# Performance work log

Hardware: AMD Instinct MI355X
Metric: run time of the kernel (lower is better)

The kernel has to match this reference:

```python
import jax, jax.numpy as jnp
import numpy as np


def setup_inputs() -> dict:
    key = jax.random.key(0)
    ks = jax.random.split(key, 9)
    B, C, O, T, H, W = 2, 256, 256, 16, 64, 64
    fea_th = jax.random.normal(ks[0], (B, C, T, H), dtype=jnp.float32)
    fea_tw = jax.random.normal(ks[1], (B, C, T, W), dtype=jnp.float32)
    fea_obj = jax.random.normal(ks[2], (B, C, T), dtype=jnp.float32)
    heatmap = jax.random.uniform(ks[3], (B, 1, T, H, W), dtype=jnp.float32)
    mask = jax.random.uniform(ks[4], (B, 1, T, H, W), dtype=jnp.float32)
    s = 1.0 / np.sqrt(C)
    W3d = jax.random.uniform(ks[5], (O, C), dtype=jnp.float32, minval=-s, maxval=s)
    b3d = jax.random.uniform(ks[6], (O,), dtype=jnp.float32, minval=-s, maxval=s)
    W1d = jax.random.uniform(ks[7], (O, C), dtype=jnp.float32, minval=-s, maxval=s)
    b1d = jax.random.uniform(ks[8], (O,), dtype=jnp.float32, minval=-s, maxval=s)
    return {"fea_th": fea_th, "fea_tw": fea_tw, "fea_obj": fea_obj,
            "heatmap": heatmap, "mask": mask,
            "W3d": W3d, "b3d": b3d, "W1d": W1d, "b1d": b1d}


def reference(fea_th, fea_tw, fea_obj, heatmap, mask, W3d, b3d, W1d, b1d):
    # Outer product over spatial dims: [B,C,T,H,1] * [B,C,T,1,W] -> [B,C,T,H,W]
    out_fea = fea_th[..., None] * fea_tw[..., None, :]
    # 1x1x1 Conv3d == channel mixing: bcthw,oc -> bothw (+ bias)
    out_fea = jnp.einsum('bcthw,oc->bothw', out_fea, W3d) + b3d[None, :, None, None, None]
    # 1x1 Conv1d on fea_obj: bct,oc -> bot (+ bias), then broadcast over H,W
    fea_obj_ = (jnp.einsum('bct,oc->bot', fea_obj, W1d) + b1d[None, :, None])[..., None, None]
    # Heatmap blend and mask
    out_fea = out_fea * (1.0 - heatmap) + fea_obj_ * heatmap
    out_fea = out_fea * mask
    return out_fea
```

## Files before the change

kernel.cpp:

```cpp
#include <hip/hip_runtime.h>
#include <hip/hip_bf16.h>

#define B_ 2
#define C_ 256
#define O_ 256
#define T_ 16
#define H_ 64
#define W_ 64

typedef __bf16 bf16x8 __attribute__((ext_vector_type(8)));
typedef float  f32x4  __attribute__((ext_vector_type(4)));

#define WS_OBJ_OFF 131072

__global__ __launch_bounds__(256) void prep_kernel(
    const float* __restrict__ fea_obj, const float* __restrict__ W3d,
    const float* __restrict__ W1d, const float* __restrict__ b1d,
    __bf16* __restrict__ wsW, float* __restrict__ wsObj) {
    const int bid = blockIdx.x;
    const int tid = threadIdx.x;
    if (bid < 32) {
        const int b = bid >> 4, t = bid & 15;
        __shared__ float fo[C_];
        fo[tid] = fea_obj[(b * C_ + tid) * T_ + t];
        __syncthreads();
        const int o = tid;
        const float4* wrow = (const float4*)(W1d + o * C_);
        float s = 0.f;
#pragma unroll 8
        for (int cq = 0; cq < C_ / 4; ++cq) {
            float4 wv = wrow[cq];
            s += wv.x * fo[cq * 4 + 0] + wv.y * fo[cq * 4 + 1] +
                 wv.z * fo[cq * 4 + 2] + wv.w * fo[cq * 4 + 3];
        }
        wsObj[(b * T_ + t) * O_ + o] = s + b1d[o];
    } else {
        const int g = (bid - 32) * 256 + tid;
        const int o = g >> 5;
        const int cg = g & 31;
        const float* sp = W3d + o * C_ + cg * 8;
        float4 a0 = *(const float4*)sp;
        float4 a1 = *(const float4*)(sp + 4);
        bf16x8 pk;
        pk[0] = (__bf16)a0.x; pk[1] = (__bf16)a0.y;
        pk[2] = (__bf16)a0.z; pk[3] = (__bf16)a0.w;
        pk[4] = (__bf16)a1.x; pk[5] = (__bf16)a1.y;
        pk[6] = (__bf16)a1.z; pk[7] = (__bf16)a1.w;
        *(bf16x8*)((char*)wsW + o * 512 + cg * 16) = pk;
    }
}

__global__ __attribute__((amdgpu_flat_work_group_size(512, 512)))
void main_kernel(
    const float* __restrict__ fea_th, const float* __restrict__ fea_tw,
    const float* __restrict__ heatmap, const float* __restrict__ mask,
    const float* __restrict__ b3d,
    const __bf16* __restrict__ wsW, const float* __restrict__ wsObj,
    float* __restrict__ out) {
    __shared__ __align__(16) char smem[43008];
    char*  sB0  = smem;
    char*  sB1  = smem + 16384;
    float* sTh  = (float*)(smem + 32768);
    float* sPb  = (float*)(smem + 40960);
    float* sObj = (float*)(smem + 41984);

    const int tid  = threadIdx.x;
    const int lane = tid & 63;
    const int wv   = tid >> 6;
    const int kgrp = lane >> 4;
    const int l15  = lane & 15;

    const int bid = blockIdx.x;
    const int wb = bid & 1, hg = (bid >> 1) & 7, bt = bid >> 4;
    const int b = bt >> 4, t = bt & 15;
    const int h0 = hg * 8, w0 = wb * 32;

    const float* objp = wsObj + (b * T_ + t) * O_;
    if (tid < 256) {
        const float* thp = fea_th + ((b * C_ + tid) * T_ + t) * H_ + h0;
        float4 v0 = *(const float4*)thp;
        float4 v1 = *(const float4*)(thp + 4);
        sTh[0 * 256 + tid] = v0.x;  sTh[1 * 256 + tid] = v0.y;
        sTh[2 * 256 + tid] = v0.z;  sTh[3 * 256 + tid] = v0.w;
        sTh[4 * 256 + tid] = v1.x;  sTh[5 * 256 + tid] = v1.y;
        sTh[6 * 256 + tid] = v1.z;  sTh[7 * 256 + tid] = v1.w;
        sPb[tid]  = b3d[tid];
        sObj[tid] = objp[tid];
    }

    const int wl = tid & 31;
    const int cs = (tid >> 5) * 16;
    bf16x8 twb0, twb1;
    {
        const float* twp = fea_tw + ((b * C_ + cs) * T_ + t) * W_ + w0 + wl;
#pragma unroll
        for (int j = 0; j < 8; ++j) twb0[j] = (__bf16)twp[j * (T_ * W_)];
#pragma unroll
        for (int j = 0; j < 8; ++j) twb1[j] = (__bf16)twp[(8 + j) * (T_ * W_)];
    }

    bf16x8 af[2][8];
#pragma unroll
    for (int mf = 0; mf < 2; ++mf)
#pragma unroll
        for (int ks = 0; ks < 8; ++ks)
            af[mf][ks] = *(const bf16x8*)(
                wsW + (wv * 32 + mf * 16 + l15) * 256 + ks * 32 + kgrp * 8);

    const int swzW = (wl & 7) << 4;
    const int c0g  = (cs >> 3) * 16;

    auto build = [&](int hl, char* dst) {
        const float* thp = sTh + hl * 256 + cs;
        const f32x4 t0 = *(const f32x4*)thp;
        const f32x4 t1 = *(const f32x4*)(thp + 4);
        const f32x4 t2 = *(const f32x4*)(thp + 8);
        const f32x4 t3 = *(const f32x4*)(thp + 12);
        bf16x8 z0, z1;
        z0[0] = (__bf16)((float)twb0[0] * t0[0]);
        z0[1] = (__bf16)((float)twb0[1] * t0[1]);
        z0[2] = (__bf16)((float)twb0[2] * t0[2]);
        z0[3] = (__bf16)((float)twb0[3] * t0[3]);
        z0[4] = (__bf16)((float)twb0[4] * t1[0]);
        z0[5] = (__bf16)((float)twb0[5] * t1[1]);
        z0[6] = (__bf16)((float)twb0[6] * t1[2]);
        z0[7] = (__bf16)((float)twb0[7] * t1[3]);
        z1[0] = (__bf16)((float)twb1[0] * t2[0]);
        z1[1] = (__bf16)((float)twb1[1] * t2[1]);
        z1[2] = (__bf16)((float)twb1[2] * t2[2]);
        z1[3] = (__bf16)((float)twb1[3] * t2[3]);
        z1[4] = (__bf16)((float)twb1[4] * t3[0]);
        z1[5] = (__bf16)((float)twb1[5] * t3[1]);
        z1[6] = (__bf16)((float)twb1[6] * t3[2]);
        z1[7] = (__bf16)((float)twb1[7] * t3[3]);
        *(bf16x8*)(dst + wl * 512 + (c0g ^ swzW))        = z0;
        *(bf16x8*)(dst + wl * 512 + ((c0g + 16) ^ swzW)) = z1;
    };

    __syncthreads();
    build(0, sB0);
    __syncthreads();

    const int hmb  = (b * T_ + t) * (H_ * W_);
    const int swzR = (l15 & 7) << 4;
    const int ob0  = wv * 32 + kgrp * 4;

    for (int hl = 0; hl < 8; ++hl) {
        char* cur = (hl & 1) ? sB1 : sB0;
        if (hl < 7) build(hl + 1, (hl & 1) ? sB0 : sB1);

        const int hglb = h0 + hl;
        const int hrow = hmb + hglb * W_ + w0 + l15;
        const float ht0 = heatmap[hrow],      mk0 = mask[hrow];
        const float ht1 = heatmap[hrow + 16], mk1 = mask[hrow + 16];

        f32x4 acc[2][2] = {};
#pragma unroll
        for (int ks = 0; ks < 8; ++ks) {
            const int kb = ks * 64 + kgrp * 16;
            const bf16x8 b0 = *(const bf16x8*)(cur + l15 * 512 + (kb ^ swzR));
            const bf16x8 b1 = *(const bf16x8*)(cur + (16 + l15) * 512 + (kb ^ swzR));
            acc[0][0] = __builtin_amdgcn_mfma_f32_16x16x32_bf16(af[0][ks], b0, acc[0][0], 0, 0, 0);
            acc[0][1] = __builtin_amdgcn_mfma_f32_16x16x32_bf16(af[0][ks], b1, acc[0][1], 0, 0, 0);
            acc[1][0] = __builtin_amdgcn_mfma_f32_16x16x32_bf16(af[1][ks], b0, acc[1][0], 0, 0, 0);
            acc[1][1] = __builtin_amdgcn_mfma_f32_16x16x32_bf16(af[1][ks], b1, acc[1][1], 0, 0, 0);
        }

#pragma unroll
        for (int mf = 0; mf < 2; ++mf) {
            const f32x4 pb4 = *(const f32x4*)(sPb + ob0 + mf * 16);
            const f32x4 po4 = *(const f32x4*)(sObj + ob0 + mf * 16);
#pragma unroll
            for (int r = 0; r < 4; ++r) {
                const int o = ob0 + mf * 16 + r;
                float* orow = out + (((size_t)(b * O_ + o) * T_ + t) * H_ + hglb) * W_ + w0;
                float v0 = acc[mf][0][r] + pb4[r];
                v0 = v0 * (1.f - ht0) + po4[r] * ht0;
                orow[l15] = v0 * mk0;
                float v1 = acc[mf][1][r] + pb4[r];
                v1 = v1 * (1.f - ht1) + po4[r] * ht1;
                orow[16 + l15] = v1 * mk1;
            }
        }
        __syncthreads();
    }
}

extern "C" void kernel_launch(void* const* d_in, const int* in_sizes, int n_in,
                              void* d_out, int out_size, void* d_ws, size_t ws_size,
                              hipStream_t stream) {
    const float* fea_th  = (const float*)d_in[0];
    const float* fea_tw  = (const float*)d_in[1];
    const float* fea_obj = (const float*)d_in[2];
    const float* heatmap = (const float*)d_in[3];
    const float* mask    = (const float*)d_in[4];
    const float* W3d     = (const float*)d_in[5];
    const float* b3d     = (const float*)d_in[6];
    const float* W1d     = (const float*)d_in[7];
    const float* b1d     = (const float*)d_in[8];
    float* out = (float*)d_out;

    __bf16* wsW  = (__bf16*)d_ws;
    float* wsObj = (float*)((char*)d_ws + WS_OBJ_OFF);

    hipLaunchKernelGGL(prep_kernel, dim3(64), dim3(256), 0, stream,
                       fea_obj, W3d, W1d, b1d, wsW, wsObj);
    hipLaunchKernelGGL(main_kernel, dim3(512), dim3(512), 0, stream,
                       fea_th, fea_tw, heatmap, mask, b3d, wsW, wsObj, out);
}
```

Measured before the change: 48.25 us.

## Fuse prep kernel into main kernel and use nontemporal loads/stores

Removes the separate prep kernel. Each block now converts W3d rows to bf16 in registers itself and computes the Conv1d object projection for its (b,t) into shared memory. This drops a launch and the workspace round trip. In exchange, the W1d GEMV and the W3d conversion are repeated across all 512 blocks. Heatmap and mask loads and the output stores now use nontemporal hints, and the loop barrier becomes a custom LDS waitcnt plus s_barrier with a sched_barrier.

```diff
diff --git a/kernel.cpp b/kernel.cpp
--- a/kernel.cpp
+++ b/kernel.cpp
@@ -11,58 +11,27 @@
 typedef __bf16 bf16x8 __attribute__((ext_vector_type(8)));
 typedef float  f32x4  __attribute__((ext_vector_type(4)));
 
-#define WS_OBJ_OFF 131072
-
-__global__ __launch_bounds__(256) void prep_kernel(
-    const float* __restrict__ fea_obj, const float* __restrict__ W3d,
-    const float* __restrict__ W1d, const float* __restrict__ b1d,
-    __bf16* __restrict__ wsW, float* __restrict__ wsObj) {
-    const int bid = blockIdx.x;
-    const int tid = threadIdx.x;
-    if (bid < 32) {
-        const int b = bid >> 4, t = bid & 15;
-        __shared__ float fo[C_];
-        fo[tid] = fea_obj[(b * C_ + tid) * T_ + t];
-        __syncthreads();
-        const int o = tid;
-        const float4* wrow = (const float4*)(W1d + o * C_);
-        float s = 0.f;
-#pragma unroll 8
-        for (int cq = 0; cq < C_ / 4; ++cq) {
-            float4 wv = wrow[cq];
-            s += wv.x * fo[cq * 4 + 0] + wv.y * fo[cq * 4 + 1] +
-                 wv.z * fo[cq * 4 + 2] + wv.w * fo[cq * 4 + 3];
-        }
-        wsObj[(b * T_ + t) * O_ + o] = s + b1d[o];
-    } else {
-        const int g = (bid - 32) * 256 + tid;
-        const int o = g >> 5;
-        const int cg = g & 31;
-        const float* sp = W3d + o * C_ + cg * 8;
-        float4 a0 = *(const float4*)sp;
-        float4 a1 = *(const float4*)(sp + 4);
-        bf16x8 pk;
-        pk[0] = (__bf16)a0.x; pk[1] = (__bf16)a0.y;
-        pk[2] = (__bf16)a0.z; pk[3] = (__bf16)a0.w;
-        pk[4] = (__bf16)a1.x; pk[5] = (__bf16)a1.y;
-        pk[6] = (__bf16)a1.z; pk[7] = (__bf16)a1.w;
-        *(bf16x8*)((char*)wsW + o * 512 + cg * 16) = pk;
-    }
+__device__ __forceinline__ void barrier_lds() {
+    asm volatile("s_waitcnt lgkmcnt(0)" ::: "memory");
+    __builtin_amdgcn_s_barrier();
+    __builtin_amdgcn_sched_barrier(0);
 }
 
 __global__ __attribute__((amdgpu_flat_work_group_size(512, 512)))
-void main_kernel(
+void fused_kernel(
     const float* __restrict__ fea_th, const float* __restrict__ fea_tw,
+    const float* __restrict__ fea_obj,
     const float* __restrict__ heatmap, const float* __restrict__ mask,
-    const float* __restrict__ b3d,
-    const __bf16* __restrict__ wsW, const float* __restrict__ wsObj,
+    const float* __restrict__ W3d, const float* __restrict__ b3d,
+    const float* __restrict__ W1d, const float* __restrict__ b1d,
     float* __restrict__ out) {
-    __shared__ __align__(16) char smem[43008];
+    __shared__ __align__(16) char smem[44032];
     char*  sB0  = smem;
     char*  sB1  = smem + 16384;
     float* sTh  = (float*)(smem + 32768);
     float* sPb  = (float*)(smem + 40960);
     float* sObj = (float*)(smem + 41984);
+    float* sFo  = (float*)(smem + 43008);
 
     const int tid  = threadIdx.x;
     const int lane = tid & 63;
@@ -75,7 +44,6 @@
     const int b = bt >> 4, t = bt & 15;
     const int h0 = hg * 8, w0 = wb * 32;
 
-    const float* objp = wsObj + (b * T_ + t) * O_;
     if (tid < 256) {
         const float* thp = fea_th + ((b * C_ + tid) * T_ + t) * H_ + h0;
         float4 v0 = *(const float4*)thp;
@@ -84,8 +52,8 @@
         sTh[2 * 256 + tid] = v0.z;  sTh[3 * 256 + tid] = v0.w;
         sTh[4 * 256 + tid] = v1.x;  sTh[5 * 256 + tid] = v1.y;
         sTh[6 * 256 + tid] = v1.z;  sTh[7 * 256 + tid] = v1.w;
-        sPb[tid]  = b3d[tid];
-        sObj[tid] = objp[tid];
+        sFo[tid] = fea_obj[(b * C_ + tid) * T_ + t];
+        sPb[tid] = b3d[tid];
     }
 
     const int wl = tid & 31;
@@ -103,12 +71,21 @@
 #pragma unroll
     for (int mf = 0; mf < 2; ++mf)
 #pragma unroll
-        for (int ks = 0; ks < 8; ++ks)
-            af[mf][ks] = *(const bf16x8*)(
-                wsW + (wv * 32 + mf * 16 + l15) * 256 + ks * 32 + kgrp * 8);
+        for (int ks = 0; ks < 8; ++ks) {
+            const float* wp = W3d + (wv * 32 + mf * 16 + l15) * C_ +
+                              ks * 32 + kgrp * 8;
+            const f32x4 a0 = *(const f32x4*)wp;
+            const f32x4 a1 = *(const f32x4*)(wp + 4);
+            bf16x8 pk;
+            pk[0] = (__bf16)a0[0]; pk[1] = (__bf16)a0[1];
+            pk[2] = (__bf16)a0[2]; pk[3] = (__bf16)a0[3];
+            pk[4] = (__bf16)a1[0]; pk[5] = (__bf16)a1[1];
+            pk[6] = (__bf16)a1[2]; pk[7] = (__bf16)a1[3];
+            af[mf][ks] = pk;
+        }
 
     const int swzW = (wl & 7) << 4;
-    const int c0g  = (cs >> 3) * 16;
+    const int c0g  = cs * 2;
 
     auto build = [&](int hl, char* dst) {
         const float* thp = sTh + hl * 256 + cs;
@@ -138,6 +115,19 @@
     };
 
     __syncthreads();
+
+    if (tid < 256) {
+        const float4* wrow = (const float4*)(W1d + tid * C_);
+        float s = 0.f;
+#pragma unroll 8
+        for (int cq = 0; cq < C_ / 4; ++cq) {
+            const float4 w4 = wrow[cq];
+            s += w4.x * sFo[cq * 4 + 0] + w4.y * sFo[cq * 4 + 1] +
+                 w4.z * sFo[cq * 4 + 2] + w4.w * sFo[cq * 4 + 3];
+        }
+        sObj[tid] = s + b1d[tid];
+    }
+
     build(0, sB0);
     __syncthreads();
 
@@ -151,8 +141,10 @@
 
         const int hglb = h0 + hl;
         const int hrow = hmb + hglb * W_ + w0 + l15;
-        const float ht0 = heatmap[hrow],      mk0 = mask[hrow];
-        const float ht1 = heatmap[hrow + 16], mk1 = mask[hrow + 16];
+        const float ht0 = __builtin_nontemporal_load(heatmap + hrow);
+        const float mk0 = __builtin_nontemporal_load(mask + hrow);
+        const float ht1 = __builtin_nontemporal_load(heatmap + hrow + 16);
+        const float mk1 = __builtin_nontemporal_load(mask + hrow + 16);
 
         f32x4 acc[2][2] = {};
 #pragma unroll
@@ -176,13 +168,13 @@
                 float* orow = out + (((size_t)(b * O_ + o) * T_ + t) * H_ + hglb) * W_ + w0;
                 float v0 = acc[mf][0][r] + pb4[r];
                 v0 = v0 * (1.f - ht0) + po4[r] * ht0;
-                orow[l15] = v0 * mk0;
+                __builtin_nontemporal_store(v0 * mk0, orow + l15);
                 float v1 = acc[mf][1][r] + pb4[r];
                 v1 = v1 * (1.f - ht1) + po4[r] * ht1;
-                orow[16 + l15] = v1 * mk1;
+                __builtin_nontemporal_store(v1 * mk1, orow + 16 + l15);
             }
         }
-        __syncthreads();
+        barrier_lds();
     }
 }
 
@@ -200,11 +192,7 @@
     const float* b1d     = (const float*)d_in[8];
     float* out = (float*)d_out;
 
-    __bf16* wsW  = (__bf16*)d_ws;
-    float* wsObj = (float*)((char*)d_ws + WS_OBJ_OFF);
-
-    hipLaunchKernelGGL(prep_kernel, dim3(64), dim3(256), 0, stream,
-                       fea_obj, W3d, W1d, b1d, wsW, wsObj);
-    hipLaunchKernelGGL(main_kernel, dim3(512), dim3(512), 0, stream,
-                       fea_th, fea_tw, heatmap, mask, b3d, wsW, wsObj, out);
+    hipLaunchKernelGGL(fused_kernel, dim3(512), dim3(512), 0, stream,
+                       fea_th, fea_tw, fea_obj, heatmap, mask,
+                       W3d, b3d, W1d, b1d, out);
 }
```

Result: slower. 72.04 us (+49.3%).
